# Kernel optimization log

Hardware: AMD Instinct MI355X
Metric: run time of the kernel (lower is better)

Reference implementation:

```python
import jax, jax.numpy as jnp
import numpy as np

TOP_K = 2


def setup_inputs() -> dict:
    key = jax.random.key(0)
    k1, k2 = jax.random.split(key)
    hidden_states = jax.random.normal(k1, (4, 8192, 4096), dtype=jnp.float32)
    # xavier_uniform for Linear(4096 -> 64): bound = sqrt(6/(fan_in+fan_out))
    bound = float(np.sqrt(6.0 / (4096 + 64)))
    gate_w = jax.random.uniform(k2, (64, 4096), dtype=jnp.float32, minval=-bound, maxval=bound)
    return {"hidden_states": hidden_states, "gate_w": gate_w}


def reference(hidden_states, gate_w):
    # Flatten [B, S, H] -> [T, H]
    H = hidden_states.shape[-1]
    x = hidden_states.reshape(-1, H)
    # Gate projection: [T, H] @ [H, E] -> [T, E]
    router_logits = jnp.einsum('th,eh->te', x, gate_w)
    # Top-k expert selection (eval mode: no noise)
    top_k_logits, top_k_indices = jax.lax.top_k(router_logits, TOP_K)
    # Normalize selected weights with a softmax over the k logits
    top_k_weights = jax.nn.softmax(top_k_logits, axis=-1)
    return top_k_weights, top_k_indices, router_logits
```

## Files before the change

### kernel.cpp

```cpp
#include <hip/hip_runtime.h>


#define NT   256
#define TT   32768
#define HD   4096
#define NE   64
#define BMT  64
#define BKT  32
#define NKT  (HD / BKT)

typedef __attribute__((ext_vector_type(8))) short bf16x8;
typedef __attribute__((ext_vector_type(4))) float f32x4;

#define MFMA __builtin_amdgcn_mfma_f32_16x16x32_bf16

__device__ __forceinline__ void tsplit8(float4 a, float4 b,
                                        uint4& o0, uint4& o1, uint4& o2) {
  float f[8] = {a.x, a.y, a.z, a.w, b.x, b.y, b.z, b.w};
  unsigned p0[4], p1[4], p2[4];
#pragma unroll
  for (int j = 0; j < 4; ++j) {
    float x0 = f[2 * j], x1 = f[2 * j + 1];
    unsigned u0 = __float_as_uint(x0) & 0xffff0000u;
    unsigned u1 = __float_as_uint(x1) & 0xffff0000u;
    float r0 = x0 - __uint_as_float(u0);
    float r1 = x1 - __uint_as_float(u1);
    unsigned v0 = __float_as_uint(r0) & 0xffff0000u;
    unsigned v1 = __float_as_uint(r1) & 0xffff0000u;
    float s0 = r0 - __uint_as_float(v0);
    float s1 = r1 - __uint_as_float(v1);
    p0[j] = (u0 >> 16) | u1;
    p1[j] = (v0 >> 16) | v1;
    p2[j] = (__float_as_uint(s0) >> 16) | (__float_as_uint(s1) & 0xffff0000u);
  }
  o0 = make_uint4(p0[0], p0[1], p0[2], p0[3]);
  o1 = make_uint4(p1[0], p1[1], p1[2], p1[3]);
  o2 = make_uint4(p2[0], p2[1], p2[2], p2[3]);
}


__global__ __launch_bounds__(NT, 2)
void topk_router_kernel(const float* __restrict__ A, const float* __restrict__ W,
                        float* __restrict__ outw, float* __restrict__ outi,
                        float* __restrict__ outl) {
  __shared__ __align__(16) unsigned char smem[49152];

  const int tid  = threadIdx.x;
  const int bm   = blockIdx.x;
  const int lane = tid & 63;
  const int wid  = tid >> 6;
  const int wr   = wid >> 1;
  const int wc   = wid & 1;
  const int l15  = lane & 15;
  const int lg   = lane >> 4;

  const int s_r  = tid >> 2;
  const int s_cb = (tid & 3) << 3;

  const float* aball = A + (size_t)(bm * BMT + s_r) * HD + s_cb;
  const float* bball = W + (size_t)s_r * HD + s_cb;

  const unsigned wswz  = ((unsigned)((s_r >> 1) & 3)) << 4;
  const unsigned wbyte = (unsigned)(s_r * 64) + (((unsigned)(s_cb * 2)) ^ wswz);

  f32x4 acc00 = {0.f,0.f,0.f,0.f}, acc01 = {0.f,0.f,0.f,0.f};
  f32x4 acc10 = {0.f,0.f,0.f,0.f}, acc11 = {0.f,0.f,0.f,0.f};

  float4 aE0, aE1, bE0, bE1;
  float4 aO0, aO1, bO0, bO1;

#define LOADS(T, A0, A1, B0, B1) { \
    const float4* ap = (const float4*)(aball + (size_t)(T) * BKT); \
    A0 = ap[0]; A1 = ap[1]; \
    const float4* bp = (const float4*)(bball + (size_t)(T) * BKT); \
    B0 = bp[0]; B1 = bp[1]; }

#define CONVW(BB, A0, A1, B0, B1) { \
    uint4 o0, o1, o2; \
    tsplit8(A0, A1, o0, o1, o2); \
    *(uint4*)(smem + (BB) +     0 + wbyte) = o0; \
    *(uint4*)(smem + (BB) +  4096 + wbyte) = o1; \
    *(uint4*)(smem + (BB) +  8192 + wbyte) = o2; \
    tsplit8(B0, B1, o0, o1, o2); \
    *(uint4*)(smem + (BB) + 12288 + wbyte) = o0; \
    *(uint4*)(smem + (BB) + 16384 + wbyte) = o1; \
    *(uint4*)(smem + (BB) + 20480 + wbyte) = o2; }

  auto compute = [&](int bb) {
    bf16x8 a0m0, a0m1, a1m0, a1m1, a2m0, a2m1;
    bf16x8 b0n0, b0n1, b1n0, b1n1, b2n0, b2n1;
    const unsigned kb = (unsigned)(lg * 16);
#define LDA(SI, MI, DST) { \
    int row = wr * 32 + (MI) * 16 + l15; \
    DST = *(const bf16x8*)(smem + bb + (SI) * 4096 + row * 64 + \
          (kb ^ ((((unsigned)row >> 1) & 3) << 4))); }
#define LDB(SI, NI, DST) { \
    int row = wc * 32 + (NI) * 16 + l15; \
    DST = *(const bf16x8*)(smem + bb + 12288 + (SI) * 4096 + row * 64 + \
          (kb ^ ((((unsigned)row >> 1) & 3) << 4))); }
    LDA(0, 0, a0m0) LDA(0, 1, a0m1)
    LDA(1, 0, a1m0) LDA(1, 1, a1m1)
    LDA(2, 0, a2m0) LDA(2, 1, a2m1)
    LDB(0, 0, b0n0) LDB(0, 1, b0n1)
    LDB(1, 0, b1n0) LDB(1, 1, b1n1)
    LDB(2, 0, b2n0) LDB(2, 1, b2n1)
#undef LDA
#undef LDB
#define PROD(AI, BI) \
    acc00 = MFMA(a##AI##m0, b##BI##n0, acc00, 0, 0, 0); \
    acc01 = MFMA(a##AI##m0, b##BI##n1, acc01, 0, 0, 0); \
    acc10 = MFMA(a##AI##m1, b##BI##n0, acc10, 0, 0, 0); \
    acc11 = MFMA(a##AI##m1, b##BI##n1, acc11, 0, 0, 0);
    PROD(0, 2) PROD(1, 1) PROD(2, 0) PROD(0, 1) PROD(1, 0) PROD(0, 0)
#undef PROD
  };

  LOADS(0, aE0, aE1, bE0, bE1)
  LOADS(1, aO0, aO1, bO0, bO1)
  CONVW(0, aE0, aE1, bE0, bE1)
  __syncthreads();

#pragma unroll 1
  for (int kk = 0; kk < NKT; kk += 2) {
    if (kk + 2 < NKT) { LOADS(kk + 2, aE0, aE1, bE0, bE1) }
    __builtin_amdgcn_sched_barrier(0);
    compute(0);
    CONVW(24576, aO0, aO1, bO0, bO1)
    __syncthreads();
    if (kk + 3 < NKT) { LOADS(kk + 3, aO0, aO1, bO0, bO1) }
    __builtin_amdgcn_sched_barrier(0);
    compute(24576);
    if (kk + 2 < NKT) { CONVW(0, aE0, aE1, bE0, bE1) }
    __syncthreads();
  }

  const int t0 = bm * BMT;
  float* lf = (float*)smem;

#define EPI(MI, NI, ACC) \
  { _Pragma("unroll") \
    for (int r = 0; r < 4; ++r) { \
      int tl = wr * 32 + (MI) * 16 + lg * 4 + r; \
      int e  = wc * 32 + (NI) * 16 + l15; \
      float v = ACC[r]; \
      outl[(size_t)(t0 + tl) * NE + e] = v; \
      lf[tl * 65 + e] = v; \
    } }
  EPI(0, 0, acc00) EPI(0, 1, acc01) EPI(1, 0, acc10) EPI(1, 1, acc11)
#undef EPI

  __syncthreads();

  if (tid < BMT) {
    const int t = tid;
    float m1 = -1e30f, m2 = -1e30f;
    int i1 = 0, i2 = 0;
#pragma unroll
    for (int e = 0; e < NE; ++e) {
      float v = lf[t * 65 + e];
      if (v > m1)      { m2 = m1; i2 = i1; m1 = v; i1 = e; }
      else if (v > m2) { m2 = v; i2 = e; }
    }
    float e2  = expf(m2 - m1);
    float inv = 1.0f / (1.0f + e2);
    outw[(size_t)(t0 + t) * 2 + 0] = inv;
    outw[(size_t)(t0 + t) * 2 + 1] = e2 * inv;
    outi[(size_t)(t0 + t) * 2 + 0] = (float)i1;
    outi[(size_t)(t0 + t) * 2 + 1] = (float)i2;
  }
}

extern "C" void kernel_launch(void* const* d_in, const int* in_sizes, int n_in,
                              void* d_out, int out_size, void* d_ws, size_t ws_size,
                              hipStream_t stream) {
  (void)in_sizes; (void)n_in; (void)d_ws; (void)ws_size; (void)out_size;
  const float* A = (const float*)d_in[0];
  const float* W = (const float*)d_in[1];
  float* outw = (float*)d_out;
  float* outi = (float*)d_out + 2 * TT;
  float* outl = (float*)d_out + 4 * TT;

  dim3 grid(TT / BMT);
  dim3 block(NT);
  hipLaunchKernelGGL(topk_router_kernel, grid, block, 0, stream, A, W, outw, outi, outl);
}
```

Measured before the change: 168.5 us.

## Pre-split gate weights into bf16 limbs and load operands directly without LDS

Adds a small pre-pass that splits the gate weights into three bf16 limbs once, stored in workspace. The main kernel then loads A straight from global memory into MFMA operand registers, splitting it in registers, and reads the pre-split W limbs directly, skipping the LDS staging and the per-block W conversion. This removes LDS traffic and the per-iteration __syncthreads. In exchange there is an extra launch, and W and A reads are no longer coalesced through shared memory, so each wave re-reads operands from L2. The old LDS kernel is kept as a fallback when the workspace is too small.

```diff
diff --git a/kernel.cpp b/kernel.cpp
--- a/kernel.cpp
+++ b/kernel.cpp
@@ -8,11 +8,16 @@
 #define BMT  64
 #define BKT  32
 #define NKT  (HD / BKT)
+#define WLIMB (NE * HD)
 
 typedef __attribute__((ext_vector_type(8))) short bf16x8;
 typedef __attribute__((ext_vector_type(4))) float f32x4;
 
 #define MFMA __builtin_amdgcn_mfma_f32_16x16x32_bf16
+
+__device__ __forceinline__ bf16x8 u2b(uint4 u) {
+  return __builtin_bit_cast(bf16x8, u);
+}
 
 __device__ __forceinline__ void tsplit8(float4 a, float4 b,
                                         uint4& o0, uint4& o1, uint4& o2) {
@@ -38,12 +43,23 @@
   o2 = make_uint4(p2[0], p2[1], p2[2], p2[3]);
 }
 
+__global__ __launch_bounds__(256)
+void presplit_w_kernel(const float* __restrict__ W, uint4* __restrict__ Wl) {
+  const int t = blockIdx.x * 256 + threadIdx.x;
+  const float4* wp = (const float4*)W + 2 * (size_t)t;
+  float4 v0 = wp[0], v1 = wp[1];
+  uint4 o0, o1, o2;
+  tsplit8(v0, v1, o0, o1, o2);
+  Wl[t]                   = o0;
+  Wl[t + WLIMB / 8]       = o1;
+  Wl[t + 2 * (WLIMB / 8)] = o2;
+}
 
 __global__ __launch_bounds__(NT, 2)
-void topk_router_kernel(const float* __restrict__ A, const float* __restrict__ W,
-                        float* __restrict__ outw, float* __restrict__ outi,
-                        float* __restrict__ outl) {
-  __shared__ __align__(16) unsigned char smem[49152];
+void router_direct_kernel(const float* __restrict__ A, const ushort* __restrict__ Wl,
+                          float* __restrict__ outw, float* __restrict__ outi,
+                          float* __restrict__ outl) {
+  __shared__ float lf[BMT * 65];
 
   const int tid  = threadIdx.x;
   const int bm   = blockIdx.x;
@@ -54,27 +70,128 @@
   const int l15  = lane & 15;
   const int lg   = lane >> 4;
 
+  const int r0 = bm * BMT + wr * 32;
+  const int e0 = wc * 32;
+
+  const float* pa0 = A + (size_t)(r0 + l15) * HD + lg * 8;
+  const float* pa1 = pa0 + (size_t)16 * HD;
+  const ushort* pb0 = Wl + (size_t)(e0 + l15) * HD + lg * 8;
+  const ushort* pb1 = pb0 + (size_t)16 * HD;
+
+  f32x4 acc00 = {0.f,0.f,0.f,0.f}, acc01 = {0.f,0.f,0.f,0.f};
+  f32x4 acc10 = {0.f,0.f,0.f,0.f}, acc11 = {0.f,0.f,0.f,0.f};
+
+  float4 aE00, aE01, aE10, aE11, aO00, aO01, aO10, aO11;
+  bf16x8 bE00, bE01, bE02, bE10, bE11, bE12;
+  bf16x8 bO00, bO01, bO02, bO10, bO11, bO12;
+
+#define LOADA(K, S) { \
+    const float4* p0 = (const float4*)(pa0 + (size_t)(K) * BKT); \
+    const float4* p1 = (const float4*)(pa1 + (size_t)(K) * BKT); \
+    a##S##00 = p0[0]; a##S##01 = p0[1]; \
+    a##S##10 = p1[0]; a##S##11 = p1[1]; }
+
+#define LOADB(K, S) { \
+    const ushort* q0 = pb0 + (size_t)(K) * BKT; \
+    const ushort* q1 = pb1 + (size_t)(K) * BKT; \
+    b##S##00 = *(const bf16x8*)(q0); \
+    b##S##01 = *(const bf16x8*)(q0 + WLIMB); \
+    b##S##02 = *(const bf16x8*)(q0 + 2 * WLIMB); \
+    b##S##10 = *(const bf16x8*)(q1); \
+    b##S##11 = *(const bf16x8*)(q1 + WLIMB); \
+    b##S##12 = *(const bf16x8*)(q1 + 2 * WLIMB); }
+
+#define PROD1(AM0, AM1, BS0, BS1) \
+    acc00 = MFMA(AM0, BS0, acc00, 0, 0, 0); \
+    acc01 = MFMA(AM0, BS1, acc01, 0, 0, 0); \
+    acc10 = MFMA(AM1, BS0, acc10, 0, 0, 0); \
+    acc11 = MFMA(AM1, BS1, acc11, 0, 0, 0);
+
+#define STEP(S) { \
+    uint4 x0, x1, x2, y0, y1, y2; \
+    tsplit8(a##S##00, a##S##01, x0, x1, x2); \
+    tsplit8(a##S##10, a##S##11, y0, y1, y2); \
+    const bf16x8 a00 = u2b(x0), a01 = u2b(x1), a02 = u2b(x2); \
+    const bf16x8 a10 = u2b(y0), a11 = u2b(y1), a12 = u2b(y2); \
+    PROD1(a00, a10, b##S##02, b##S##12) \
+    PROD1(a01, a11, b##S##01, b##S##11) \
+    PROD1(a02, a12, b##S##00, b##S##10) \
+    PROD1(a00, a10, b##S##01, b##S##11) \
+    PROD1(a01, a11, b##S##00, b##S##10) \
+    PROD1(a00, a10, b##S##00, b##S##10) }
+
+  LOADA(0, E) LOADB(0, E)
+#pragma unroll 1
+  for (int kt = 0; kt < NKT; kt += 2) {
+    LOADA(kt + 1, O) LOADB(kt + 1, O)
+    STEP(E)
+    if (kt + 2 < NKT) { LOADA(kt + 2, E) LOADB(kt + 2, E) }
+    STEP(O)
+    __builtin_amdgcn_s_barrier();
+  }
+
+  const int t0 = bm * BMT;
+
+#define EPI(MI, NI, ACC) \
+  { _Pragma("unroll") \
+    for (int r = 0; r < 4; ++r) { \
+      int tl = wr * 32 + (MI) * 16 + lg * 4 + r; \
+      int e  = wc * 32 + (NI) * 16 + l15; \
+      float v = ACC[r]; \
+      outl[(size_t)(t0 + tl) * NE + e] = v; \
+      lf[tl * 65 + e] = v; \
+    } }
+  EPI(0, 0, acc00) EPI(0, 1, acc01) EPI(1, 0, acc10) EPI(1, 1, acc11)
+#undef EPI
+
+  __syncthreads();
+
+  if (tid < BMT) {
+    const int t = tid;
+    float m1 = -1e30f, m2 = -1e30f;
+    int i1 = 0, i2 = 0;
+#pragma unroll
+    for (int e = 0; e < NE; ++e) {
+      float v = lf[t * 65 + e];
+      if (v > m1)      { m2 = m1; i2 = i1; m1 = v; i1 = e; }
+      else if (v > m2) { m2 = v; i2 = e; }
+    }
+    float e2  = expf(m2 - m1);
+    float inv = 1.0f / (1.0f + e2);
+    outw[(size_t)(t0 + t) * 2 + 0] = inv;
+    outw[(size_t)(t0 + t) * 2 + 1] = e2 * inv;
+    outi[(size_t)(t0 + t) * 2 + 0] = (float)i1;
+    outi[(size_t)(t0 + t) * 2 + 1] = (float)i2;
+  }
+}
+
+__global__ __launch_bounds__(NT, 2)
+void topk_router_lds(const float* __restrict__ A, const float* __restrict__ W,
+                     float* __restrict__ outw, float* __restrict__ outi,
+                     float* __restrict__ outl) {
+  __shared__ __align__(16) unsigned char smem[49152];
+  const int tid  = threadIdx.x;
+  const int bm   = blockIdx.x;
+  const int lane = tid & 63;
+  const int wid  = tid >> 6;
+  const int wr   = wid >> 1;
+  const int wc   = wid & 1;
+  const int l15  = lane & 15;
+  const int lg   = lane >> 4;
   const int s_r  = tid >> 2;
   const int s_cb = (tid & 3) << 3;
-
   const float* aball = A + (size_t)(bm * BMT + s_r) * HD + s_cb;
   const float* bball = W + (size_t)s_r * HD + s_cb;
-
   const unsigned wswz  = ((unsigned)((s_r >> 1) & 3)) << 4;
   const unsigned wbyte = (unsigned)(s_r * 64) + (((unsigned)(s_cb * 2)) ^ wswz);
-
   f32x4 acc00 = {0.f,0.f,0.f,0.f}, acc01 = {0.f,0.f,0.f,0.f};
   f32x4 acc10 = {0.f,0.f,0.f,0.f}, acc11 = {0.f,0.f,0.f,0.f};
-
-  float4 aE0, aE1, bE0, bE1;
-  float4 aO0, aO1, bO0, bO1;
-
+  float4 aE0, aE1, bE0, bE1, aO0, aO1, bO0, bO1;
 #define LOADS(T, A0, A1, B0, B1) { \
     const float4* ap = (const float4*)(aball + (size_t)(T) * BKT); \
     A0 = ap[0]; A1 = ap[1]; \
     const float4* bp = (const float4*)(bball + (size_t)(T) * BKT); \
     B0 = bp[0]; B1 = bp[1]; }
-
 #define CONVW(BB, A0, A1, B0, B1) { \
     uint4 o0, o1, o2; \
     tsplit8(A0, A1, o0, o1, o2); \
@@ -85,7 +202,6 @@
     *(uint4*)(smem + (BB) + 12288 + wbyte) = o0; \
     *(uint4*)(smem + (BB) + 16384 + wbyte) = o1; \
     *(uint4*)(smem + (BB) + 20480 + wbyte) = o2; }
-
   auto compute = [&](int bb) {
     bf16x8 a0m0, a0m1, a1m0, a1m1, a2m0, a2m1;
     bf16x8 b0n0, b0n1, b1n0, b1n1, b2n0, b2n1;
@@ -106,20 +222,17 @@
     LDB(2, 0, b2n0) LDB(2, 1, b2n1)
 #undef LDA
 #undef LDB
-#define PROD(AI, BI) \
-    acc00 = MFMA(a##AI##m0, b##BI##n0, acc00, 0, 0, 0); \
-    acc01 = MFMA(a##AI##m0, b##BI##n1, acc01, 0, 0, 0); \
-    acc10 = MFMA(a##AI##m1, b##BI##n0, acc10, 0, 0, 0); \
-    acc11 = MFMA(a##AI##m1, b##BI##n1, acc11, 0, 0, 0);
-    PROD(0, 2) PROD(1, 1) PROD(2, 0) PROD(0, 1) PROD(1, 0) PROD(0, 0)
-#undef PROD
+    PROD1(a0m0, a0m1, b2n0, b2n1)
+    PROD1(a1m0, a1m1, b1n0, b1n1)
+    PROD1(a2m0, a2m1, b0n0, b0n1)
+    PROD1(a0m0, a0m1, b1n0, b1n1)
+    PROD1(a1m0, a1m1, b0n0, b0n1)
+    PROD1(a0m0, a0m1, b0n0, b0n1)
   };
-
   LOADS(0, aE0, aE1, bE0, bE1)
   LOADS(1, aO0, aO1, bO0, bO1)
   CONVW(0, aE0, aE1, bE0, bE1)
   __syncthreads();
-
 #pragma unroll 1
   for (int kk = 0; kk < NKT; kk += 2) {
     if (kk + 2 < NKT) { LOADS(kk + 2, aE0, aE1, bE0, bE1) }
@@ -133,10 +246,8 @@
     if (kk + 2 < NKT) { CONVW(0, aE0, aE1, bE0, bE1) }
     __syncthreads();
   }
-
   const int t0 = bm * BMT;
-  float* lf = (float*)smem;
-
+  float* lf2 = (float*)smem;
 #define EPI(MI, NI, ACC) \
   { _Pragma("unroll") \
     for (int r = 0; r < 4; ++r) { \
@@ -144,20 +255,18 @@
       int e  = wc * 32 + (NI) * 16 + l15; \
       float v = ACC[r]; \
       outl[(size_t)(t0 + tl) * NE + e] = v; \
-      lf[tl * 65 + e] = v; \
+      lf2[tl * 65 + e] = v; \
     } }
   EPI(0, 0, acc00) EPI(0, 1, acc01) EPI(1, 0, acc10) EPI(1, 1, acc11)
 #undef EPI
-
   __syncthreads();
-
   if (tid < BMT) {
     const int t = tid;
     float m1 = -1e30f, m2 = -1e30f;
     int i1 = 0, i2 = 0;
 #pragma unroll
     for (int e = 0; e < NE; ++e) {
-      float v = lf[t * 65 + e];
+      float v = lf2[t * 65 + e];
       if (v > m1)      { m2 = m1; i2 = i1; m1 = v; i1 = e; }
       else if (v > m2) { m2 = v; i2 = e; }
     }
@@ -173,14 +282,21 @@
 extern "C" void kernel_launch(void* const* d_in, const int* in_sizes, int n_in,
                               void* d_out, int out_size, void* d_ws, size_t ws_size,
                               hipStream_t stream) {
-  (void)in_sizes; (void)n_in; (void)d_ws; (void)ws_size; (void)out_size;
+  (void)in_sizes; (void)n_in; (void)out_size;
   const float* A = (const float*)d_in[0];
   const float* W = (const float*)d_in[1];
   float* outw = (float*)d_out;
   float* outi = (float*)d_out + 2 * TT;
   float* outl = (float*)d_out + 4 * TT;
 
-  dim3 grid(TT / BMT);
-  dim3 block(NT);
-  hipLaunchKernelGGL(topk_router_kernel, grid, block, 0, stream, A, W, outw, outi, outl);
-}
+  const size_t need = (size_t)3 * WLIMB * sizeof(ushort);
+  if (ws_size >= need) {
+    hipLaunchKernelGGL(presplit_w_kernel, dim3(128), dim3(256), 0, stream,
+                       W, (uint4*)d_ws);
+    hipLaunchKernelGGL(router_direct_kernel, dim3(TT / BMT), dim3(NT), 0, stream,
+                       A, (const ushort*)d_ws, outw, outi, outl);
+  } else {
+    hipLaunchKernelGGL(topk_router_lds, dim3(TT / BMT), dim3(NT), 0, stream,
+                       A, W, outw, outi, outl);
+  }
+}
```

Measured after the change: 349.3 us. 2.07x slower.

## Prepack gate weights into MFMA fragment layout and load activations directly to registers

Applied to the files above, without the earlier changes.

Adds a prepass kernel that splits the gate weights into three bf16 parts once per call and stores them in MFMA fragment order in the workspace. The main kernel now processes 128 tokens per block with 512 threads and reads activation fragments straight from global memory into registers, with no LDS staging. Only the prepacked weights are double-buffered through LDS. This removes the per-block weight split and the LDS round trip for activations, at the cost of an extra launch and less coalesced direct activation loads. The old kernel is kept as a fallback when the workspace is too small.

```diff
diff --git a/kernel.cpp b/kernel.cpp
--- a/kernel.cpp
+++ b/kernel.cpp
@@ -1,18 +1,25 @@
 #include <hip/hip_runtime.h>
 
 
-#define NT   256
-#define TT   32768
-#define HD   4096
-#define NE   64
-#define BMT  64
-#define BKT  32
-#define NKT  (HD / BKT)
+#define NT    512
+#define TT    32768
+#define HD    4096
+#define NE    64
+#define BKT   32
+#define NKT   128
+#define KCH   2
+#define NCH   (NKT / KCH)
+#define BROWS 128
+#define LDSBUF_U4 1536
 
 typedef __attribute__((ext_vector_type(8))) short bf16x8;
 typedef __attribute__((ext_vector_type(4))) float f32x4;
 
 #define MFMA __builtin_amdgcn_mfma_f32_16x16x32_bf16
+
+__device__ __forceinline__ bf16x8 u2b(uint4 u) {
+  return __builtin_bit_cast(bf16x8, u);
+}
 
 __device__ __forceinline__ void tsplit8(float4 a, float4 b,
                                         uint4& o0, uint4& o1, uint4& o2) {
@@ -38,13 +45,143 @@
   o2 = make_uint4(p2[0], p2[1], p2[2], p2[3]);
 }
 
+__global__ __launch_bounds__(256)
+void prepack_w_kernel(const float* __restrict__ W, uint4* __restrict__ Bp) {
+  const int t  = blockIdx.x * 256 + threadIdx.x;
+  const int e  = t >> 9;
+  const int c8 = t & 511;
+  const int k0 = c8 * 8;
+  const float4* wp = (const float4*)(W + (size_t)e * HD + k0);
+  uint4 o0, o1, o2;
+  tsplit8(wp[0], wp[1], o0, o1, o2);
+  const int ts = k0 >> 5;
+  const int lg = (k0 >> 3) & 3;
+  const int f  = e >> 4;
+  const int ln = lg * 16 + (e & 15);
+  Bp[(((ts * 3 + 0) * 4 + f) << 6) + ln] = o0;
+  Bp[(((ts * 3 + 1) * 4 + f) << 6) + ln] = o1;
+  Bp[(((ts * 3 + 2) * 4 + f) << 6) + ln] = o2;
+}
 
 __global__ __launch_bounds__(NT, 2)
-void topk_router_kernel(const float* __restrict__ A, const float* __restrict__ W,
+void router_frag_kernel(const float* __restrict__ A, const uint4* __restrict__ Bp,
                         float* __restrict__ outw, float* __restrict__ outi,
                         float* __restrict__ outl) {
+  __shared__ __align__(16) uint4 smem[2 * LDSBUF_U4];
+
+  const int tid  = threadIdx.x;
+  const int bm   = blockIdx.x;
+  const int lane = tid & 63;
+  const int w    = tid >> 6;
+  const int l15  = lane & 15;
+  const int lg   = lane >> 4;
+
+  const int row = bm * BROWS + w * 16 + l15;
+  const float* pa = A + (size_t)row * HD + lg * 8;
+
+  const uint4* bsrc = Bp + w * 192 + lane;
+
+  f32x4 acc0 = {0.f,0.f,0.f,0.f}, acc1 = {0.f,0.f,0.f,0.f};
+  f32x4 acc2 = {0.f,0.f,0.f,0.f}, acc3 = {0.f,0.f,0.f,0.f};
+
+  uint4 st0, st1, st2;
+
+#define SLOAD(CH) { \
+    const uint4* q_ = bsrc + (size_t)(CH) * LDSBUF_U4; \
+    st0 = q_[0]; st1 = q_[64]; st2 = q_[128]; }
+
+#define SWRITE(BUFI) { \
+    uint4* d_ = smem + (BUFI) * LDSBUF_U4 + w * 192 + lane; \
+    d_[0] = st0; d_[64] = st1; d_[128] = st2; }
+
+#define FRAG(T4, F, ACC, A0_, A1_, A2_) { \
+    const bf16x8 q0_ = bbx[(((T4) * 3 + 0) * 4 + (F)) * 64 + lane]; \
+    const bf16x8 q1_ = bbx[(((T4) * 3 + 1) * 4 + (F)) * 64 + lane]; \
+    const bf16x8 q2_ = bbx[(((T4) * 3 + 2) * 4 + (F)) * 64 + lane]; \
+    ACC = MFMA(A0_, q2_, ACC, 0, 0, 0); \
+    ACC = MFMA(A1_, q1_, ACC, 0, 0, 0); \
+    ACC = MFMA(A2_, q0_, ACC, 0, 0, 0); \
+    ACC = MFMA(A0_, q1_, ACC, 0, 0, 0); \
+    ACC = MFMA(A1_, q0_, ACC, 0, 0, 0); \
+    ACC = MFMA(A0_, q0_, ACC, 0, 0, 0); }
+
+#define STEP(T4, AX0, AX1, AY0, AY1) { \
+    int tn_ = t0s + (T4) + 1; if (tn_ >= NKT) tn_ = NKT - 1; \
+    const float4* ap_ = (const float4*)(pa + (size_t)tn_ * BKT); \
+    AY0 = ap_[0]; AY1 = ap_[1]; \
+    uint4 x0_, x1_, x2_; \
+    tsplit8(AX0, AX1, x0_, x1_, x2_); \
+    const bf16x8 a0_ = u2b(x0_), a1_ = u2b(x1_), a2_ = u2b(x2_); \
+    FRAG(T4, 0, acc0, a0_, a1_, a2_) \
+    FRAG(T4, 1, acc1, a0_, a1_, a2_) \
+    FRAG(T4, 2, acc2, a0_, a1_, a2_) \
+    FRAG(T4, 3, acc3, a0_, a1_, a2_) }
+
+  SLOAD(0)
+  SWRITE(0)
+  float4 aX0, aX1, aY0, aY1;
+  { const float4* ap = (const float4*)pa; aX0 = ap[0]; aX1 = ap[1]; }
+  __syncthreads();
+
+#pragma unroll 1
+  for (int c = 0; c < NCH; ++c) {
+    const bf16x8* bbx = (const bf16x8*)(smem + (c & 1) * LDSBUF_U4);
+    const int t0s = c * KCH;
+    const bool more = (c + 1 < NCH);
+    if (more) { SLOAD(c + 1) }
+    __builtin_amdgcn_sched_barrier(0);
+    STEP(0, aX0, aX1, aY0, aY1)
+    STEP(1, aY0, aY1, aX0, aX1)
+    if (more) { SWRITE((c + 1) & 1) }
+    __syncthreads();
+  }
+
+  const int tb = bm * BROWS;
+  float* lf = (float*)smem;
+  const int rbase = w * 16 + lg * 4;
+
+#define EPO(F, ACC) { \
+    _Pragma("unroll") \
+    for (int r = 0; r < 4; ++r) { \
+      int tl = rbase + r; int e = (F) * 16 + l15; float v = ACC[r]; \
+      outl[(size_t)(tb + tl) * NE + e] = v; \
+      lf[tl * 65 + e] = v; \
+    } }
+  EPO(0, acc0) EPO(1, acc1) EPO(2, acc2) EPO(3, acc3)
+#undef EPO
+
+  __syncthreads();
+
+  if (tid < BROWS) {
+    const int t = tid;
+    float m1 = -1e30f, m2 = -1e30f;
+    int i1 = 0, i2 = 0;
+#pragma unroll
+    for (int e = 0; e < NE; ++e) {
+      float v = lf[t * 65 + e];
+      if (v > m1)      { m2 = m1; i2 = i1; m1 = v; i1 = e; }
+      else if (v > m2) { m2 = v; i2 = e; }
+    }
+    float e2  = expf(m2 - m1);
+    float inv = 1.0f / (1.0f + e2);
+    outw[(size_t)(tb + t) * 2 + 0] = inv;
+    outw[(size_t)(tb + t) * 2 + 1] = e2 * inv;
+    outi[(size_t)(tb + t) * 2 + 0] = (float)i1;
+    outi[(size_t)(tb + t) * 2 + 1] = (float)i2;
+  }
+}
+
+#define PROD1(AM0, AM1, BS0, BS1) \
+    acc00 = MFMA(AM0, BS0, acc00, 0, 0, 0); \
+    acc01 = MFMA(AM0, BS1, acc01, 0, 0, 0); \
+    acc10 = MFMA(AM1, BS0, acc10, 0, 0, 0); \
+    acc11 = MFMA(AM1, BS1, acc11, 0, 0, 0);
+
+__global__ __launch_bounds__(256, 2)
+void topk_router_lds(const float* __restrict__ A, const float* __restrict__ W,
+                     float* __restrict__ outw, float* __restrict__ outi,
+                     float* __restrict__ outl) {
   __shared__ __align__(16) unsigned char smem[49152];
-
   const int tid  = threadIdx.x;
   const int bm   = blockIdx.x;
   const int lane = tid & 63;
@@ -53,29 +190,21 @@
   const int wc   = wid & 1;
   const int l15  = lane & 15;
   const int lg   = lane >> 4;
-
   const int s_r  = tid >> 2;
   const int s_cb = (tid & 3) << 3;
-
-  const float* aball = A + (size_t)(bm * BMT + s_r) * HD + s_cb;
+  const float* aball = A + (size_t)(bm * 64 + s_r) * HD + s_cb;
   const float* bball = W + (size_t)s_r * HD + s_cb;
-
   const unsigned wswz  = ((unsigned)((s_r >> 1) & 3)) << 4;
   const unsigned wbyte = (unsigned)(s_r * 64) + (((unsigned)(s_cb * 2)) ^ wswz);
-
   f32x4 acc00 = {0.f,0.f,0.f,0.f}, acc01 = {0.f,0.f,0.f,0.f};
   f32x4 acc10 = {0.f,0.f,0.f,0.f}, acc11 = {0.f,0.f,0.f,0.f};
-
-  float4 aE0, aE1, bE0, bE1;
-  float4 aO0, aO1, bO0, bO1;
-
+  float4 aE0, aE1, bE0, bE1, aO0, aO1, bO0, bO1;
 #define LOADS(T, A0, A1, B0, B1) { \
     const float4* ap = (const float4*)(aball + (size_t)(T) * BKT); \
     A0 = ap[0]; A1 = ap[1]; \
     const float4* bp = (const float4*)(bball + (size_t)(T) * BKT); \
     B0 = bp[0]; B1 = bp[1]; }
-
-#define CONVW(BB, A0, A1, B0, B1) { \
+#define CONVW2(BB, A0, A1, B0, B1) { \
     uint4 o0, o1, o2; \
     tsplit8(A0, A1, o0, o1, o2); \
     *(uint4*)(smem + (BB) +     0 + wbyte) = o0; \
@@ -85,7 +214,6 @@
     *(uint4*)(smem + (BB) + 12288 + wbyte) = o0; \
     *(uint4*)(smem + (BB) + 16384 + wbyte) = o1; \
     *(uint4*)(smem + (BB) + 20480 + wbyte) = o2; }
-
   auto compute = [&](int bb) {
     bf16x8 a0m0, a0m1, a1m0, a1m1, a2m0, a2m1;
     bf16x8 b0n0, b0n1, b1n0, b1n1, b2n0, b2n1;
@@ -106,37 +234,32 @@
     LDB(2, 0, b2n0) LDB(2, 1, b2n1)
 #undef LDA
 #undef LDB
-#define PROD(AI, BI) \
-    acc00 = MFMA(a##AI##m0, b##BI##n0, acc00, 0, 0, 0); \
-    acc01 = MFMA(a##AI##m0, b##BI##n1, acc01, 0, 0, 0); \
-    acc10 = MFMA(a##AI##m1, b##BI##n0, acc10, 0, 0, 0); \
-    acc11 = MFMA(a##AI##m1, b##BI##n1, acc11, 0, 0, 0);
-    PROD(0, 2) PROD(1, 1) PROD(2, 0) PROD(0, 1) PROD(1, 0) PROD(0, 0)
-#undef PROD
+    PROD1(a0m0, a0m1, b2n0, b2n1)
+    PROD1(a1m0, a1m1, b1n0, b1n1)
+    PROD1(a2m0, a2m1, b0n0, b0n1)
+    PROD1(a0m0, a0m1, b1n0, b1n1)
+    PROD1(a1m0, a1m1, b0n0, b0n1)
+    PROD1(a0m0, a0m1, b0n0, b0n1)
   };
-
   LOADS(0, aE0, aE1, bE0, bE1)
   LOADS(1, aO0, aO1, bO0, bO1)
-  CONVW(0, aE0, aE1, bE0, bE1)
+  CONVW2(0, aE0, aE1, bE0, bE1)
   __syncthreads();
-
 #pragma unroll 1
   for (int kk = 0; kk < NKT; kk += 2) {
     if (kk + 2 < NKT) { LOADS(kk + 2, aE0, aE1, bE0, bE1) }
     __builtin_amdgcn_sched_barrier(0);
     compute(0);
-    CONVW(24576, aO0, aO1, bO0, bO1)
+    CONVW2(24576, aO0, aO1, bO0, bO1)
     __syncthreads();
     if (kk + 3 < NKT) { LOADS(kk + 3, aO0, aO1, bO0, bO1) }
     __builtin_amdgcn_sched_barrier(0);
     compute(24576);
-    if (kk + 2 < NKT) { CONVW(0, aE0, aE1, bE0, bE1) }
+    if (kk + 2 < NKT) { CONVW2(0, aE0, aE1, bE0, bE1) }
     __syncthreads();
   }
-
-  const int t0 = bm * BMT;
-  float* lf = (float*)smem;
-
+  const int t0 = bm * 64;
+  float* lf2 = (float*)smem;
 #define EPI(MI, NI, ACC) \
   { _Pragma("unroll") \
     for (int r = 0; r < 4; ++r) { \
@@ -144,20 +267,18 @@
       int e  = wc * 32 + (NI) * 16 + l15; \
       float v = ACC[r]; \
       outl[(size_t)(t0 + tl) * NE + e] = v; \
-      lf[tl * 65 + e] = v; \
+      lf2[tl * 65 + e] = v; \
     } }
   EPI(0, 0, acc00) EPI(0, 1, acc01) EPI(1, 0, acc10) EPI(1, 1, acc11)
 #undef EPI
-
   __syncthreads();
-
-  if (tid < BMT) {
+  if (tid < 64) {
     const int t = tid;
     float m1 = -1e30f, m2 = -1e30f;
     int i1 = 0, i2 = 0;
 #pragma unroll
     for (int e = 0; e < NE; ++e) {
-      float v = lf[t * 65 + e];
+      float v = lf2[t * 65 + e];
       if (v > m1)      { m2 = m1; i2 = i1; m1 = v; i1 = e; }
       else if (v > m2) { m2 = v; i2 = e; }
     }
@@ -173,14 +294,21 @@
 extern "C" void kernel_launch(void* const* d_in, const int* in_sizes, int n_in,
                               void* d_out, int out_size, void* d_ws, size_t ws_size,
                               hipStream_t stream) {
-  (void)in_sizes; (void)n_in; (void)d_ws; (void)ws_size; (void)out_size;
+  (void)in_sizes; (void)n_in; (void)out_size;
   const float* A = (const float*)d_in[0];
   const float* W = (const float*)d_in[1];
   float* outw = (float*)d_out;
   float* outi = (float*)d_out + 2 * TT;
   float* outl = (float*)d_out + 4 * TT;
 
-  dim3 grid(TT / BMT);
-  dim3 block(NT);
-  hipLaunchKernelGGL(topk_router_kernel, grid, block, 0, stream, A, W, outw, outi, outl);
-}
+  const size_t need = (size_t)NKT * 3 * 4 * 1024;
+  if (ws_size >= need) {
+    hipLaunchKernelGGL(prepack_w_kernel, dim3(128), dim3(256), 0, stream,
+                       W, (uint4*)d_ws);
+    hipLaunchKernelGGL(router_frag_kernel, dim3(TT / BROWS), dim3(NT), 0, stream,
+                       A, (const uint4*)d_ws, outw, outi, outl);
+  } else {
+    hipLaunchKernelGGL(topk_router_lds, dim3(TT / 64), dim3(256), 0, stream,
+                       A, W, outw, outi, outl);
+  }
+}
```

New measurement: 197.5 us. 17.2% more time.
